# Kernel tuning notes

Measured on AMD Instinct MI355X. Metric: run time of the kernel, lower is better.

## Reference

```python
import jax, jax.numpy as jnp
import numpy as np

L, D, H, V, T_BLK, B, T = 6, 768, 12, 32000, 1024, 4, 1024
HD = D // H          # head size = 64
FF = 4 * D           # FFN hidden
EPS = 1e-5


def _ln(x, g, b):
    m = x.mean(-1, keepdims=True)
    v = ((x - m) ** 2).mean(-1, keepdims=True)
    return (x - m) * jax.lax.rsqrt(v + EPS) * g + b


def _attn(q_in, kv_in, wqkv, wo, bo, causal):
    # wqkv: [3, D, D]; heads batched (equivalent to concat of per-head Linear outputs)
    Bq, Tq, _ = q_in.shape
    Tk = kv_in.shape[1]
    q = (q_in @ wqkv[0]).reshape(Bq, Tq, H, HD)
    k = (kv_in @ wqkv[1]).reshape(Bq, Tk, H, HD)
    v = (kv_in @ wqkv[2]).reshape(Bq, Tk, H, HD)
    wei = jnp.einsum('bqhd,bkhd->bhqk', q, k) * (HD ** -0.5)
    if causal:
        mask = jnp.tril(jnp.ones((Tq, Tk), dtype=bool))
        wei = jnp.where(mask, wei, -jnp.inf)
    wei = jax.nn.softmax(wei, axis=-1)
    out = jnp.einsum('bhqk,bkhd->bqhd', wei, v).reshape(Bq, Tq, D)
    return out @ wo + bo


def _ffn(x, w1, b1, w2, b2):
    return jax.nn.relu(x @ w1 + b1) @ w2 + b2


def _forward(idx, encoder_input,
             enc_tok, enc_pos, enc_qkv, enc_wo, enc_bo, enc_w1, enc_b1, enc_w2, enc_b2,
             enc_ln1g, enc_ln1b, enc_ln2g, enc_ln2b, enc_lnfg, enc_lnfb,
             dec_tok, dec_pos, dec_qkv, dec_wo, dec_bo, dec_cqkv, dec_cwo, dec_cbo,
             dec_w1, dec_b1, dec_w2, dec_b2,
             dec_ln1g, dec_ln1b, dec_ln2g, dec_ln2b, dec_ln3g, dec_ln3b,
             dec_lnfg, dec_lnfb, lm_w, lm_b):
    # ---- encoder (NOTE: original Head always applies causal tril, so encoder is causal) ----
    Te = encoder_input.shape[1]
    x = enc_tok[encoder_input] + enc_pos[:Te]
    for i in range(L):
        h = _ln(x, enc_ln1g[i], enc_ln1b[i])
        x = x + _attn(h, h, enc_qkv[i], enc_wo[i], enc_bo[i], causal=True)
        h = _ln(x, enc_ln2g[i], enc_ln2b[i])
        x = x + _ffn(h, enc_w1[i], enc_b1[i], enc_w2[i], enc_b2[i])
    enc_out = _ln(x, enc_lnfg, enc_lnfb)
    # ---- decoder ----
    Td = idx.shape[1]
    y = dec_tok[idx] + dec_pos[:Td]
    for i in range(L):
        h = _ln(y, dec_ln1g[i], dec_ln1b[i])
        y = y + _attn(h, h, dec_qkv[i], dec_wo[i], dec_bo[i], causal=True)
        h = _ln(y, dec_ln2g[i], dec_ln2b[i])
        y = y + _attn(h, enc_out, dec_cqkv[i], dec_cwo[i], dec_cbo[i], causal=False)
        h = _ln(y, dec_ln3g[i], dec_ln3b[i])
        y = y + _ffn(h, dec_w1[i], dec_b1[i], dec_w2[i], dec_b2[i])
    y = _ln(y, dec_lnfg, dec_lnfb)
    return y @ lm_w + lm_b  # logits [B, T, V]


def setup_inputs() -> dict:
    key = jax.random.key(0)
    keys = iter(jax.random.split(key, 80))
    def nrm(shape, s=0.02):
        return jax.random.normal(next(keys), shape, dtype=jnp.float32) * s
    z = lambda shape: jnp.zeros(shape, jnp.float32)
    o = lambda shape: jnp.ones(shape, jnp.float32)
    inp = {}
    inp['idx'] = jax.random.randint(next(keys), (B, T), 0, V)
    inp['encoder_input'] = jax.random.randint(next(keys), (B, T), 0, V)
    # encoder params
    inp['enc_tok'] = nrm((V, D)); inp['enc_pos'] = nrm((T_BLK, D))
    inp['enc_qkv'] = nrm((L, 3, D, D)); inp['enc_wo'] = nrm((L, D, D)); inp['enc_bo'] = z((L, D))
    inp['enc_w1'] = nrm((L, D, FF)); inp['enc_b1'] = z((L, FF))
    inp['enc_w2'] = nrm((L, FF, D)); inp['enc_b2'] = z((L, D))
    inp['enc_ln1g'] = o((L, D)); inp['enc_ln1b'] = z((L, D))
    inp['enc_ln2g'] = o((L, D)); inp['enc_ln2b'] = z((L, D))
    inp['enc_lnfg'] = o((D,)); inp['enc_lnfb'] = z((D,))
    # decoder params
    inp['dec_tok'] = nrm((V, D)); inp['dec_pos'] = nrm((T_BLK, D))
    inp['dec_qkv'] = nrm((L, 3, D, D)); inp['dec_wo'] = nrm((L, D, D)); inp['dec_bo'] = z((L, D))
    inp['dec_cqkv'] = nrm((L, 3, D, D)); inp['dec_cwo'] = nrm((L, D, D)); inp['dec_cbo'] = z((L, D))
    inp['dec_w1'] = nrm((L, D, FF)); inp['dec_b1'] = z((L, FF))
    inp['dec_w2'] = nrm((L, FF, D)); inp['dec_b2'] = z((L, D))
    inp['dec_ln1g'] = o((L, D)); inp['dec_ln1b'] = z((L, D))
    inp['dec_ln2g'] = o((L, D)); inp['dec_ln2b'] = z((L, D))
    inp['dec_ln3g'] = o((L, D)); inp['dec_ln3b'] = z((L, D))
    inp['dec_lnfg'] = o((D,)); inp['dec_lnfb'] = z((D,))
    inp['lm_w'] = nrm((D, V)); inp['lm_b'] = z((V,))
    return inp


def reference(idx, encoder_input,
              enc_tok, enc_pos, enc_qkv, enc_wo, enc_bo, enc_w1, enc_b1, enc_w2, enc_b2,
              enc_ln1g, enc_ln1b, enc_ln2g, enc_ln2b, enc_lnfg, enc_lnfb,
              dec_tok, dec_pos, dec_qkv, dec_wo, dec_bo, dec_cqkv, dec_cwo, dec_cbo,
              dec_w1, dec_b1, dec_w2, dec_b2,
              dec_ln1g, dec_ln1b, dec_ln2g, dec_ln2b, dec_ln3g, dec_ln3b,
              dec_lnfg, dec_lnfb, lm_w, lm_b):
    return _forward(idx, encoder_input,
                    enc_tok, enc_pos, enc_qkv, enc_wo, enc_bo, enc_w1, enc_b1, enc_w2, enc_b2,
                    enc_ln1g, enc_ln1b, enc_ln2g, enc_ln2b, enc_lnfg, enc_lnfb,
                    dec_tok, dec_pos, dec_qkv, dec_wo, dec_bo, dec_cqkv, dec_cwo, dec_cbo,
                    dec_w1, dec_b1, dec_w2, dec_b2,
                    dec_ln1g, dec_ln1b, dec_ln2g, dec_ln2b, dec_ln3g, dec_ln3b,
                    dec_lnfg, dec_lnfb, lm_w, lm_b)
```

## Files before the change

kernel.cpp:

```cpp
#include <hip/hip_runtime.h>


typedef __bf16 bf16x8 __attribute__((ext_vector_type(8)));
typedef float  f32x4  __attribute__((ext_vector_type(4)));
typedef unsigned short u16x4 __attribute__((ext_vector_type(4)));
typedef unsigned short u16x8 __attribute__((ext_vector_type(8)));

constexpr int Lc = 6, Dc = 768, Hc = 12, HDc = 64, Vc = 32000;
constexpr int Bc = 4, Tc = 1024, FFc = 3072;
constexpr int Mtot = Bc * Tc;

static __device__ __forceinline__ unsigned short f2bf(float f) {
  union { float f; unsigned u; } x; x.f = f;
  unsigned r = x.u + 0x7fffu + ((x.u >> 16) & 1u);
  return (unsigned short)(r >> 16);
}
static __device__ __forceinline__ float bf2f(unsigned short s) {
  union { unsigned u; float f; } c; c.u = (unsigned)s << 16; return c.f;
}

static __device__ __forceinline__ void gl_lds16(const unsigned short* g, unsigned short* l) {
  __builtin_amdgcn_global_load_lds(
      (const __attribute__((address_space(1))) unsigned int*)g,
      (__attribute__((address_space(3))) unsigned int*)l, 16, 0, 0);
}

template <int N> static __device__ __forceinline__ void wait_vm() {
  if constexpr (N == 0)      asm volatile("s_waitcnt vmcnt(0)" ::: "memory");
  else if constexpr (N == 3) asm volatile("s_waitcnt vmcnt(3)" ::: "memory");
  else if constexpr (N == 4) asm volatile("s_waitcnt vmcnt(4)" ::: "memory");
}

static __device__ __forceinline__ float blockReduceSum(float v, float* red) {
  #pragma unroll
  for (int o = 32; o; o >>= 1) v += __shfl_xor(v, o, 64);
  int w = threadIdx.x >> 6;
  __syncthreads();
  if ((threadIdx.x & 63) == 0) red[w] = v;
  __syncthreads();
  return red[0] + red[1] + red[2] + red[3];
}

__global__ __launch_bounds__(256) void wconv_k(const float* __restrict__ W,
                                               unsigned short* __restrict__ WT,
                                               int K, int N) {
  __shared__ float t[32][33];
  const long zoff = (long)blockIdx.z * K * N;
  const int k0 = blockIdx.x * 32, n0 = blockIdx.y * 32;
  const int tid = threadIdx.x;
  const int rr = tid >> 3;
  const int cc = (tid & 7) * 4;
  f32x4 v = *reinterpret_cast<const f32x4*>(W + zoff + (long)(k0 + rr) * N + n0 + cc);
  #pragma unroll
  for (int j = 0; j < 4; j++) t[rr][cc + j] = v[j];
  __syncthreads();
  u16x4 o;
  #pragma unroll
  for (int j = 0; j < 4; j++) o[j] = f2bf(t[cc + j][rr]);
  *reinterpret_cast<u16x4*>(WT + zoff + (long)(n0 + rr) * K + k0 + cc) = o;
}

__global__ __launch_bounds__(256) void vtrans_k(const unsigned short* __restrict__ V,
                                                unsigned short* __restrict__ VT) {
  __shared__ unsigned short t[64][65];
  const int bh = blockIdx.y;
  const int b = bh / Hc, h = bh % Hc;
  const int t0 = blockIdx.x * 64;
  const int tid = threadIdx.x;
  const int rr = tid >> 3;
  const int c8 = (tid & 7) * 8;
  #pragma unroll
  for (int rep = 0; rep < 2; rep++) {
    int row = rep * 32 + rr;
    u16x8 v = *reinterpret_cast<const u16x8*>(V + (long)(b * Tc + t0 + row) * Dc + h * HDc + c8);
    #pragma unroll
    for (int j = 0; j < 8; j++) t[row][c8 + j] = v[j];
  }
  __syncthreads();
  #pragma unroll
  for (int rep = 0; rep < 2; rep++) {
    int hd = rep * 32 + rr;
    u16x8 o;
    #pragma unroll
    for (int j = 0; j < 8; j++) o[j] = t[c8 + j][hd];
    *reinterpret_cast<u16x8*>(VT + ((long)bh * HDc + hd) * Tc + t0 + c8) = o;
  }
}

__global__ __launch_bounds__(256) void embed_k(const int* __restrict__ idx,
                                               const float* __restrict__ tok,
                                               const float* __restrict__ pos,
                                               float* __restrict__ out) {
  const long row = blockIdx.x;
  const int t = (int)(row % Tc);
  const long id = idx[row];
  #pragma unroll
  for (int j = 0; j < 3; j++) {
    int e = threadIdx.x + j * 256;
    out[row * Dc + e] = tok[id * Dc + e] + pos[(long)t * Dc + e];
  }
}

__global__ __launch_bounds__(256) void ln_k(const float* __restrict__ X,
                                            const float* __restrict__ g,
                                            const float* __restrict__ bta,
                                            unsigned short* __restrict__ out) {
  __shared__ float red[4];
  const long row = blockIdx.x;
  const int tid = threadIdx.x;
  float v[3];
  #pragma unroll
  for (int j = 0; j < 3; j++) v[j] = X[row * Dc + tid + j * 256];
  float s = v[0] + v[1] + v[2];
  s = blockReduceSum(s, red);
  float mean = s * (1.f / 768.f);
  float q = 0.f;
  #pragma unroll
  for (int j = 0; j < 3; j++) { float d = v[j] - mean; q += d * d; }
  q = blockReduceSum(q, red);
  float rstd = rsqrtf(q * (1.f / 768.f) + 1e-5f);
  #pragma unroll
  for (int j = 0; j < 3; j++) {
    int e = tid + j * 256;
    out[row * Dc + e] = f2bf((v[j] - mean) * rstd * g[e] + bta[e]);
  }
}

template <bool CAUSAL>
__global__ __launch_bounds__(256) void flash_k(
    const unsigned short* __restrict__ Q,
    const unsigned short* __restrict__ K,
    const unsigned short* __restrict__ VT,
    unsigned short* __restrict__ O) {
  __shared__ __align__(16) unsigned short Ks[128 * 64];
  __shared__ __align__(16) unsigned short Vs[64 * 128];
  __shared__ __align__(16) unsigned short Ps[4][32 * 128];

  const int tid = threadIdx.x;
  const int lane = tid & 63;
  const int w = tid >> 6;
  const int lane16 = lane & 15;
  const int l4 = lane >> 4;
  const int bh = blockIdx.y;
  const int b = bh / Hc, h = bh % Hc;
  const int q0 = blockIdx.x * 128;

  const unsigned short* Qb = Q + ((long)b * Tc) * Dc + h * HDc;
  const unsigned short* Kb = K + ((long)b * Tc) * Dc + h * HDc;
  const unsigned short* Vb = VT + (long)bh * HDc * Tc;
  unsigned short* Ob = O + ((long)b * Tc) * Dc + h * HDc;

  bf16x8 qf[2][2];
  #pragma unroll
  for (int m = 0; m < 2; m++)
    #pragma unroll
    for (int kk = 0; kk < 2; kk++) {
      u16x8 raw = *reinterpret_cast<const u16x8*>(
          Qb + (long)(q0 + w * 32 + m * 16 + lane16) * Dc + kk * 32 + l4 * 8);
      bf16x8 f;
      #pragma unroll
      for (int j = 0; j < 8; j++) f[j] = (__bf16)(bf2f(raw[j]) * 0.125f);
      qf[m][kk] = f;
    }

  float mrow[2][4], lrow[2][4];
  f32x4 accO[2][4];
  #pragma unroll
  for (int m = 0; m < 2; m++)
    #pragma unroll
    for (int r = 0; r < 4; r++) { mrow[m][r] = -1e30f; lrow[m][r] = 0.f; }
  #pragma unroll
  for (int m = 0; m < 2; m++)
    #pragma unroll
    for (int d4 = 0; d4 < 4; d4++)
      #pragma unroll
      for (int r = 0; r < 4; r++) accO[m][d4][r] = 0.f;

  const int nch = CAUSAL ? (blockIdx.x + 1) : (Tc / 128);
  for (int c = 0; c < nch; c++) {
    const int k0 = c * 128;
    __syncthreads();
    #pragma unroll
    for (int it = 0; it < 4; it++) {
      int u = (it * 4 + w) * 64 + lane;
      int r = u >> 3, s = u & 7;
      gl_lds16(Kb + (long)(k0 + r) * Dc + ((s ^ (r & 7)) * 8), &Ks[(it * 4 + w) * 512]);
      int r2 = u >> 4, s2 = u & 15;
      gl_lds16(Vb + (long)r2 * Tc + k0 + ((s2 ^ (r2 & 7)) * 8), &Vs[(it * 4 + w) * 512]);
    }
    __syncthreads();

    f32x4 sacc[2][8];
    #pragma unroll
    for (int m = 0; m < 2; m++)
      #pragma unroll
      for (int n = 0; n < 8; n++)
        #pragma unroll
        for (int r = 0; r < 4; r++) sacc[m][n][r] = 0.f;
    #pragma unroll
    for (int n = 0; n < 8; n++) {
      int row = n * 16 + lane16;
      #pragma unroll
      for (int kk = 0; kk < 2; kk++) {
        bf16x8 kf = *reinterpret_cast<const bf16x8*>(
            &Ks[row * 64 + (((kk * 4 + l4) ^ (row & 7)) * 8)]);
        sacc[0][n] = __builtin_amdgcn_mfma_f32_16x16x32_bf16(qf[0][kk], kf, sacc[0][n], 0, 0, 0);
        sacc[1][n] = __builtin_amdgcn_mfma_f32_16x16x32_bf16(qf[1][kk], kf, sacc[1][n], 0, 0, 0);
      }
    }

    if (CAUSAL && c == nch - 1) {
      #pragma unroll
      for (int m = 0; m < 2; m++)
        #pragma unroll
        for (int n = 0; n < 8; n++)
          #pragma unroll
          for (int r = 0; r < 4; r++) {
            int kcol = k0 + n * 16 + lane16;
            int q = q0 + w * 32 + m * 16 + l4 * 4 + r;
            if (kcol > q) sacc[m][n][r] = -1e30f;
          }
    }

    #pragma unroll
    for (int m = 0; m < 2; m++)
      #pragma unroll
      for (int r = 0; r < 4; r++) {
        float smax = sacc[m][0][r];
        #pragma unroll
        for (int n = 1; n < 8; n++) smax = fmaxf(smax, sacc[m][n][r]);
        #pragma unroll
        for (int off = 1; off < 16; off <<= 1) smax = fmaxf(smax, __shfl_xor(smax, off, 64));
        float mold = mrow[m][r];
        float mnew = fmaxf(mold, smax);
        float sc = __expf(mold - mnew);
        float psum = 0.f;
        unsigned short pv[8];
        #pragma unroll
        for (int n = 0; n < 8; n++) {
          float p = __expf(sacc[m][n][r] - mnew);
          psum += p;
          pv[n] = f2bf(p);
        }
        #pragma unroll
        for (int off = 1; off < 16; off <<= 1) psum += __shfl_xor(psum, off, 64);
        lrow[m][r] = lrow[m][r] * sc + psum;
        mrow[m][r] = mnew;
        #pragma unroll
        for (int d4 = 0; d4 < 4; d4++) accO[m][d4][r] *= sc;
        int prow = m * 16 + l4 * 4 + r;
        #pragma unroll
        for (int n = 0; n < 8; n++) {
          int col = n * 16 + lane16;
          Ps[w][prow * 128 + (((col >> 3) ^ (prow & 7)) * 8) + (col & 7)] = pv[n];
        }
      }

    #pragma unroll
    for (int kk = 0; kk < 4; kk++) {
      bf16x8 pa[2];
      #pragma unroll
      for (int m = 0; m < 2; m++) {
        int arow = m * 16 + lane16;
        pa[m] = *reinterpret_cast<const bf16x8*>(
            &Ps[w][arow * 128 + (((kk * 4 + l4) ^ (arow & 7)) * 8)]);
      }
      #pragma unroll
      for (int d4 = 0; d4 < 4; d4++) {
        int vrow = d4 * 16 + lane16;
        bf16x8 vf = *reinterpret_cast<const bf16x8*>(
            &Vs[vrow * 128 + (((kk * 4 + l4) ^ (vrow & 7)) * 8)]);
        accO[0][d4] = __builtin_amdgcn_mfma_f32_16x16x32_bf16(pa[0], vf, accO[0][d4], 0, 0, 0);
        accO[1][d4] = __builtin_amdgcn_mfma_f32_16x16x32_bf16(pa[1], vf, accO[1][d4], 0, 0, 0);
      }
    }
  }

  #pragma unroll
  for (int m = 0; m < 2; m++)
    #pragma unroll
    for (int r = 0; r < 4; r++) {
      float inv = 1.f / lrow[m][r];
      int q = q0 + w * 32 + m * 16 + l4 * 4 + r;
      #pragma unroll
      for (int d4 = 0; d4 < 4; d4++)
        Ob[(long)q * Dc + d4 * 16 + lane16] = f2bf(accO[m][d4][r] * inv);
    }
}

template <int BM, int BN, int MF, int NF, int MINW,
          bool HASBIAS, bool RELU, bool HASRES, bool OUTBF>
__global__ __launch_bounds__(256, MINW) void gemm_k(
    const unsigned short* __restrict__ A, long sAb, long sAh, int lda,
    const unsigned short* __restrict__ BT, long sBb, long sBh, int ldb,
    void* Cp, long sCb, long sCh, int ldc,
    const float* __restrict__ bias,
    const float* __restrict__ Res, int ldr,
    int K, int nH, float alpha) {
  constexpr int AI = BM / 64;
  constexpr int BI = BN / 64;
  constexpr int VC = AI + BI;
  __shared__ __align__(16) unsigned short As[2][BM * 32];
  __shared__ __align__(16) unsigned short Bs[2][BN * 32];

  const int tid = threadIdx.x;
  const int lane = tid & 63;
  const int w = tid >> 6;
  const int wr = w >> 1, wc = w & 1;
  const int lane16 = lane & 15;
  const int l4 = lane >> 4;

  const int z = blockIdx.z;
  const int bb = z / nH, hh = z % nH;
  const long offA = sAb * bb + sAh * hh;
  const long offB = sBb * bb + sBh * hh;
  const long offC = sCb * bb + sCh * hh;

  const int gx = gridDim.x;
  const int nwg = gx * gridDim.y;
  const int id = blockIdx.y * gx + blockIdx.x;
  const int q8 = nwg >> 3, r8 = nwg & 7;
  const int xcd = id & 7, ord = id >> 3;
  const int swz = (xcd < r8 ? xcd * (q8 + 1) : r8 * (q8 + 1) + (xcd - r8) * q8) + ord;
  const int m0 = (swz % gx) * BM;
  const int n0 = (swz / gx) * BN;

  const int srow = lane >> 2;
  const int sslot = ((lane & 3) ^ ((srow >> 1) & 3)) * 8;

  const unsigned short* aP[AI];
  #pragma unroll
  for (int j = 0; j < AI; j++)
    aP[j] = A + offA + (long)(m0 + w * (BM / 4) + j * 16 + srow) * lda + sslot;
  const unsigned short* bP[BI];
  #pragma unroll
  for (int j = 0; j < BI; j++)
    bP[j] = BT + offB + (long)(n0 + w * (BN / 4) + j * 16 + srow) * ldb + sslot;

  f32x4 acc[MF][NF];
  #pragma unroll
  for (int m = 0; m < MF; m++)
    #pragma unroll
    for (int n = 0; n < NF; n++)
      #pragma unroll
      for (int r = 0; r < 4; r++) acc[m][n][r] = 0.f;

  auto STAGE = [&](int buf, int k0) {
    #pragma unroll
    for (int j = 0; j < AI; j++)
      gl_lds16(aP[j] + k0, &As[buf][(w * (BM / 4) + j * 16) * 32]);
    #pragma unroll
    for (int j = 0; j < BI; j++)
      gl_lds16(bP[j] + k0, &Bs[buf][(w * (BN / 4) + j * 16) * 32]);
  };

  const int nt = K / 32;
  STAGE(0, 0);
  int cur = 0;
  for (int t = 0; t < nt; t++) {
    if (t + 1 < nt) { STAGE(cur ^ 1, (t + 1) * 32); wait_vm<VC>(); }
    else            { wait_vm<0>(); }
    __builtin_amdgcn_sched_barrier(0);
    __builtin_amdgcn_s_barrier();
    __builtin_amdgcn_sched_barrier(0);

    bf16x8 afr[MF], bfr[NF];
    #pragma unroll
    for (int n = 0; n < NF; n++) {
      int row = wc * NF * 16 + n * 16 + lane16;
      bfr[n] = *reinterpret_cast<const bf16x8*>(
          &Bs[cur][row * 32 + ((l4 ^ ((row >> 1) & 3)) * 8)]);
    }
    #pragma unroll
    for (int m = 0; m < MF; m++) {
      int row = wr * MF * 16 + m * 16 + lane16;
      afr[m] = *reinterpret_cast<const bf16x8*>(
          &As[cur][row * 32 + ((l4 ^ ((row >> 1) & 3)) * 8)]);
    }
    __builtin_amdgcn_s_setprio(1);
    #pragma unroll
    for (int m = 0; m < MF; m++)
      #pragma unroll
      for (int n = 0; n < NF; n++)
        acc[m][n] = __builtin_amdgcn_mfma_f32_16x16x32_bf16(afr[m], bfr[n], acc[m][n], 0, 0, 0);
    __builtin_amdgcn_s_setprio(0);

    asm volatile("s_waitcnt lgkmcnt(0)" ::: "memory");
    __builtin_amdgcn_sched_barrier(0);
    __builtin_amdgcn_s_barrier();
    cur ^= 1;
  }

  const int r0 = m0 + wr * MF * 16;
  const int c0 = n0 + wc * NF * 16;
  #pragma unroll
  for (int m = 0; m < MF; m++) {
    #pragma unroll
    for (int n = 0; n < NF; n++) {
      #pragma unroll
      for (int r = 0; r < 4; r++) {
        int rr = r0 + m * 16 + l4 * 4 + r;
        int cc = c0 + n * 16 + lane16;
        float v = acc[m][n][r] * alpha;
        if constexpr (HASBIAS) v += bias[cc];
        if constexpr (RELU) v = fmaxf(v, 0.f);
        if constexpr (HASRES) v += Res[offC + (long)rr * ldr + cc];
        if constexpr (OUTBF) ((unsigned short*)Cp)[offC + (long)rr * ldc + cc] = f2bf(v);
        else                 ((float*)Cp)[offC + (long)rr * ldc + cc] = v;
      }
    }
  }
}

extern "C" void kernel_launch(void* const* d_in, const int* in_sizes, int n_in,
                              void* d_out, int out_size, void* d_ws, size_t ws_size,
                              hipStream_t stream) {
  (void)in_sizes; (void)n_in; (void)out_size;

  const int*   idx      = (const int*)d_in[0];
  const int*   enc_in   = (const int*)d_in[1];
  const float* enc_tok  = (const float*)d_in[2];
  const float* enc_pos  = (const float*)d_in[3];
  const float* enc_qkv  = (const float*)d_in[4];
  const float* enc_wo   = (const float*)d_in[5];
  const float* enc_bo   = (const float*)d_in[6];
  const float* enc_w1   = (const float*)d_in[7];
  const float* enc_b1   = (const float*)d_in[8];
  const float* enc_w2   = (const float*)d_in[9];
  const float* enc_b2   = (const float*)d_in[10];
  const float* enc_ln1g = (const float*)d_in[11];
  const float* enc_ln1b = (const float*)d_in[12];
  const float* enc_ln2g = (const float*)d_in[13];
  const float* enc_ln2b = (const float*)d_in[14];
  const float* enc_lnfg = (const float*)d_in[15];
  const float* enc_lnfb = (const float*)d_in[16];
  const float* dec_tok  = (const float*)d_in[17];
  const float* dec_pos  = (const float*)d_in[18];
  const float* dec_qkv  = (const float*)d_in[19];
  const float* dec_wo   = (const float*)d_in[20];
  const float* dec_bo   = (const float*)d_in[21];
  const float* dec_cqkv = (const float*)d_in[22];
  const float* dec_cwo  = (const float*)d_in[23];
  const float* dec_cbo  = (const float*)d_in[24];
  const float* dec_w1   = (const float*)d_in[25];
  const float* dec_b1   = (const float*)d_in[26];
  const float* dec_w2   = (const float*)d_in[27];
  const float* dec_b2   = (const float*)d_in[28];
  const float* dec_ln1g = (const float*)d_in[29];
  const float* dec_ln1b = (const float*)d_in[30];
  const float* dec_ln2g = (const float*)d_in[31];
  const float* dec_ln2b = (const float*)d_in[32];
  const float* dec_ln3g = (const float*)d_in[33];
  const float* dec_ln3b = (const float*)d_in[34];
  const float* dec_lnfg = (const float*)d_in[35];
  const float* dec_lnfb = (const float*)d_in[36];
  const float* lm_w     = (const float*)d_in[37];
  const float* lm_b     = (const float*)d_in[38];

  constexpr long De2 = (long)Dc * Dc;
  constexpr long DF  = (long)Dc * FFc;

  unsigned short* wcache = (unsigned short*)d_out;
  size_t woff = 0;
  auto take = [&](size_t n) { unsigned short* p = wcache + woff; woff += n; return p; };
  unsigned short* enc_qkvT  = take(18ul * De2);
  unsigned short* enc_woT   = take(6ul * De2);
  unsigned short* enc_w1T   = take(6ul * DF);
  unsigned short* enc_w2T   = take(6ul * DF);
  unsigned short* dec_qkvT  = take(18ul * De2);
  unsigned short* dec_woT   = take(6ul * De2);
  unsigned short* dec_cqkvT = take(18ul * De2);
  unsigned short* dec_cwoT  = take(6ul * De2);
  unsigned short* dec_w1T   = take(6ul * DF);
  unsigned short* dec_w2T   = take(6ul * DF);

  char* ws = (char*)d_ws;
  const size_t need = (size_t)Dc * Vc * 2 + 2ull * Mtot * Dc * 4 + 3ull * Mtot * Dc * 2 +
                      3ull * Mtot * Dc * 2 + (size_t)Mtot * FFc * 2 + (size_t)Mtot * Dc * 2 +
                      (size_t)Bc * Hc * HDc * Tc * 2 + 4096;
  if (ws_size < need) return;
  auto takeW = [&](size_t bytes) { char* p = ws; ws += (bytes + 255) & ~255ull; return p; };
  unsigned short* lm_wT = (unsigned short*)takeW((size_t)Dc * Vc * 2);
  float* xe             = (float*)takeW((size_t)Mtot * Dc * 4);
  float* xd             = (float*)takeW((size_t)Mtot * Dc * 4);
  unsigned short* hbf   = (unsigned short*)takeW((size_t)Mtot * Dc * 2);
  unsigned short* qkvb  = (unsigned short*)takeW(3ull * Mtot * Dc * 2);
  unsigned short* ao    = (unsigned short*)takeW((size_t)Mtot * Dc * 2);
  unsigned short* mid   = (unsigned short*)takeW((size_t)Mtot * FFc * 2);
  unsigned short* eo    = (unsigned short*)takeW((size_t)Mtot * Dc * 2);
  unsigned short* vT    = (unsigned short*)takeW((size_t)Bc * Hc * HDc * Tc * 2);
  unsigned short* qb = qkvb;
  unsigned short* kb = qkvb + (size_t)Mtot * Dc;
  unsigned short* vb = qkvb + 2ull * Mtot * Dc;

  const dim3 TB(256);

  wconv_k<<<dim3(Dc/32, Dc/32, 18), TB, 0, stream>>>(enc_qkv, enc_qkvT, Dc, Dc);
  wconv_k<<<dim3(Dc/32, Dc/32,  6), TB, 0, stream>>>(enc_wo,  enc_woT,  Dc, Dc);
  wconv_k<<<dim3(Dc/32, FFc/32, 6), TB, 0, stream>>>(enc_w1,  enc_w1T,  Dc, FFc);
  wconv_k<<<dim3(FFc/32, Dc/32, 6), TB, 0, stream>>>(enc_w2,  enc_w2T,  FFc, Dc);
  wconv_k<<<dim3(Dc/32, Dc/32, 18), TB, 0, stream>>>(dec_qkv, dec_qkvT, Dc, Dc);
  wconv_k<<<dim3(Dc/32, Dc/32,  6), TB, 0, stream>>>(dec_wo,  dec_woT,  Dc, Dc);
  wconv_k<<<dim3(Dc/32, Dc/32, 18), TB, 0, stream>>>(dec_cqkv,dec_cqkvT,Dc, Dc);
  wconv_k<<<dim3(Dc/32, Dc/32,  6), TB, 0, stream>>>(dec_cwo, dec_cwoT, Dc, Dc);
  wconv_k<<<dim3(Dc/32, FFc/32, 6), TB, 0, stream>>>(dec_w1,  dec_w1T,  Dc, FFc);
  wconv_k<<<dim3(FFc/32, Dc/32, 6), TB, 0, stream>>>(dec_w2,  dec_w2T,  FFc, Dc);
  wconv_k<<<dim3(Dc/32, Vc/32,  1), TB, 0, stream>>>(lm_w,    lm_wT,    Dc, Vc);

  auto LN = [&](const float* X, const float* g, const float* b, unsigned short* o) {
    ln_k<<<dim3(Mtot), TB, 0, stream>>>(X, g, b, o);
  };
  auto QKV3 = [&](const unsigned short* Abf, const unsigned short* W3T) {
    gemm_k<128,128,4,4,3,false,false,false,true><<<dim3(Mtot/128, Dc/128, 3), TB, 0, stream>>>(
        Abf, 0, 0, Dc, W3T, De2, 0, Dc,
        qkvb, (long)Mtot*Dc, 0, Dc, nullptr, nullptr, 0, Dc, 1, 1.f);
  };
  auto PROJ1 = [&](const unsigned short* Abf, const unsigned short* WT, unsigned short* Cb) {
    gemm_k<128,64,4,2,4,false,false,false,true><<<dim3(Mtot/128, Dc/64, 1), TB, 0, stream>>>(
        Abf, 0, 0, Dc, WT, 0, 0, Dc,
        Cb, 0, 0, Dc, nullptr, nullptr, 0, Dc, 1, 1.f);
  };
  auto KV2 = [&](const unsigned short* Abf, const unsigned short* W2T) {
    gemm_k<128,64,4,2,4,false,false,false,true><<<dim3(Mtot/128, Dc/64, 2), TB, 0, stream>>>(
        Abf, 0, 0, Dc, W2T, De2, 0, Dc,
        kb, (long)Mtot*Dc, 0, Dc, nullptr, nullptr, 0, Dc, 1, 1.f);
  };
  auto VT = [&]() {
    vtrans_k<<<dim3(Tc/64, Bc*Hc), TB, 0, stream>>>(vb, vT);
  };
  auto FLASH = [&](bool causal) {
    if (causal) flash_k<true ><<<dim3(Tc/128, Bc*Hc), TB, 0, stream>>>(qb, kb, vT, ao);
    else        flash_k<false><<<dim3(Tc/128, Bc*Hc), TB, 0, stream>>>(qb, kb, vT, ao);
  };
  auto ORES = [&](const unsigned short* Abf, const unsigned short* WT, const float* bias, float* X) {
    gemm_k<128,64,4,2,4,true,false,true,false><<<dim3(Mtot/128, Dc/64, 1), TB, 0, stream>>>(
        Abf, 0, 0, Dc, WT, 0, 0, Dc,
        X, 0, 0, Dc, bias, X, Dc, Dc, 1, 1.f);
  };
  auto FFN1 = [&](const unsigned short* Abf, const unsigned short* WT, const float* bias) {
    gemm_k<128,128,4,4,3,true,true,false,true><<<dim3(Mtot/128, FFc/128, 1), TB, 0, stream>>>(
        Abf, 0, 0, Dc, WT, 0, 0, Dc,
        mid, 0, 0, FFc, bias, nullptr, 0, Dc, 1, 1.f);
  };
  auto FFN2 = [&](const unsigned short* WT, const float* bias, float* X) {
    gemm_k<128,64,4,2,4,true,false,true,false><<<dim3(Mtot/128, Dc/64, 1), TB, 0, stream>>>(
        mid, 0, 0, FFc, WT, 0, 0, FFc,
        X, 0, 0, Dc, bias, X, Dc, FFc, 1, 1.f);
  };

  embed_k<<<dim3(Mtot), TB, 0, stream>>>(enc_in, enc_tok, enc_pos, xe);
  for (int i = 0; i < Lc; i++) {
    LN(xe, enc_ln1g + i * Dc, enc_ln1b + i * Dc, hbf);
    QKV3(hbf, enc_qkvT + (size_t)i * 3 * De2);
    VT(); FLASH(true);
    ORES(ao, enc_woT + (size_t)i * De2, enc_bo + i * Dc, xe);
    LN(xe, enc_ln2g + i * Dc, enc_ln2b + i * Dc, hbf);
    FFN1(hbf, enc_w1T + (size_t)i * DF, enc_b1 + i * FFc);
    FFN2(enc_w2T + (size_t)i * DF, enc_b2 + i * Dc, xe);
  }
  LN(xe, enc_lnfg, enc_lnfb, eo);

  embed_k<<<dim3(Mtot), TB, 0, stream>>>(idx, dec_tok, dec_pos, xd);
  for (int i = 0; i < Lc; i++) {
    LN(xd, dec_ln1g + i * Dc, dec_ln1b + i * Dc, hbf);
    QKV3(hbf, dec_qkvT + (size_t)i * 3 * De2);
    VT(); FLASH(true);
    ORES(ao, dec_woT + (size_t)i * De2, dec_bo + i * Dc, xd);
    LN(xd, dec_ln2g + i * Dc, dec_ln2b + i * Dc, hbf);
    PROJ1(hbf, dec_cqkvT + (size_t)i * 3 * De2, qb);
    KV2(eo, dec_cqkvT + (size_t)i * 3 * De2 + De2);
    VT(); FLASH(false);
    ORES(ao, dec_cwoT + (size_t)i * De2, dec_cbo + i * Dc, xd);
    LN(xd, dec_ln3g + i * Dc, dec_ln3b + i * Dc, hbf);
    FFN1(hbf, dec_w1T + (size_t)i * DF, dec_b1 + i * FFc);
    FFN2(dec_w2T + (size_t)i * DF, dec_b2 + i * Dc, xd);
  }
  LN(xd, dec_lnfg, dec_lnfb, hbf);

  gemm_k<128,128,4,4,3,true,false,false,false><<<dim3(Mtot/128, Vc/128, 1), TB, 0, stream>>>(
      hbf, 0, 0, Dc, lm_wT, 0, 0, Dc,
      d_out, 0, 0, Vc, lm_b, nullptr, 0, Dc, 1, 1.f);
}
```

Before: 4.025 ms.

## Merge cross-attention Q/KV GEMMs, shrink GEMM tiles, nontemporal LM-head stores

```diff
diff --git a/kernel.cpp b/kernel.cpp
--- a/kernel.cpp
+++ b/kernel.cpp
@@ -27,6 +27,7 @@
 
 template <int N> static __device__ __forceinline__ void wait_vm() {
   if constexpr (N == 0)      asm volatile("s_waitcnt vmcnt(0)" ::: "memory");
+  else if constexpr (N == 2) asm volatile("s_waitcnt vmcnt(2)" ::: "memory");
   else if constexpr (N == 3) asm volatile("s_waitcnt vmcnt(3)" ::: "memory");
   else if constexpr (N == 4) asm volatile("s_waitcnt vmcnt(4)" ::: "memory");
 }
@@ -289,13 +290,14 @@
 }
 
 template <int BM, int BN, int MF, int NF, int MINW,
-          bool HASBIAS, bool RELU, bool HASRES, bool OUTBF>
+          bool HASBIAS, bool RELU, bool HASRES, bool OUTBF, bool NT>
 __global__ __launch_bounds__(256, MINW) void gemm_k(
     const unsigned short* __restrict__ A, long sAb, long sAh, int lda,
     const unsigned short* __restrict__ BT, long sBb, long sBh, int ldb,
     void* Cp, long sCb, long sCh, int ldc,
     const float* __restrict__ bias,
     const float* __restrict__ Res, int ldr,
+    const unsigned short* __restrict__ A2,
     int K, int nH, float alpha) {
   constexpr int AI = BM / 64;
   constexpr int BI = BN / 64;
@@ -312,6 +314,7 @@
 
   const int z = blockIdx.z;
   const int bb = z / nH, hh = z % nH;
+  const unsigned short* Abase = (A2 != nullptr && hh != 0) ? A2 : A;
   const long offA = sAb * bb + sAh * hh;
   const long offB = sBb * bb + sBh * hh;
   const long offC = sCb * bb + sCh * hh;
@@ -331,7 +334,7 @@
   const unsigned short* aP[AI];
   #pragma unroll
   for (int j = 0; j < AI; j++)
-    aP[j] = A + offA + (long)(m0 + w * (BM / 4) + j * 16 + srow) * lda + sslot;
+    aP[j] = Abase + offA + (long)(m0 + w * (BM / 4) + j * 16 + srow) * lda + sslot;
   const unsigned short* bP[BI];
   #pragma unroll
   for (int j = 0; j < BI; j++)
@@ -405,8 +408,13 @@
         if constexpr (HASBIAS) v += bias[cc];
         if constexpr (RELU) v = fmaxf(v, 0.f);
         if constexpr (HASRES) v += Res[offC + (long)rr * ldr + cc];
-        if constexpr (OUTBF) ((unsigned short*)Cp)[offC + (long)rr * ldc + cc] = f2bf(v);
-        else                 ((float*)Cp)[offC + (long)rr * ldc + cc] = v;
+        if constexpr (OUTBF) {
+          ((unsigned short*)Cp)[offC + (long)rr * ldc + cc] = f2bf(v);
+        } else {
+          float* dst = (float*)Cp + offC + (long)rr * ldc + cc;
+          if constexpr (NT) __builtin_nontemporal_store(v, dst);
+          else              *dst = v;
+        }
       }
     }
   }
@@ -511,19 +519,16 @@
     ln_k<<<dim3(Mtot), TB, 0, stream>>>(X, g, b, o);
   };
   auto QKV3 = [&](const unsigned short* Abf, const unsigned short* W3T) {
-    gemm_k<128,128,4,4,3,false,false,false,true><<<dim3(Mtot/128, Dc/128, 3), TB, 0, stream>>>(
-        Abf, 0, 0, Dc, W3T, De2, 0, Dc,
-        qkvb, (long)Mtot*Dc, 0, Dc, nullptr, nullptr, 0, Dc, 1, 1.f);
-  };
-  auto PROJ1 = [&](const unsigned short* Abf, const unsigned short* WT, unsigned short* Cb) {
-    gemm_k<128,64,4,2,4,false,false,false,true><<<dim3(Mtot/128, Dc/64, 1), TB, 0, stream>>>(
-        Abf, 0, 0, Dc, WT, 0, 0, Dc,
-        Cb, 0, 0, Dc, nullptr, nullptr, 0, Dc, 1, 1.f);
-  };
-  auto KV2 = [&](const unsigned short* Abf, const unsigned short* W2T) {
-    gemm_k<128,64,4,2,4,false,false,false,true><<<dim3(Mtot/128, Dc/64, 2), TB, 0, stream>>>(
-        Abf, 0, 0, Dc, W2T, De2, 0, Dc,
-        kb, (long)Mtot*Dc, 0, Dc, nullptr, nullptr, 0, Dc, 1, 1.f);
+    gemm_k<128,64,4,2,4,false,false,false,true,false>
+      <<<dim3(Mtot/128, Dc/64, 3), TB, 0, stream>>>(
+        Abf, De2 * 0 + 0, 0, Dc, W3T, De2, 0, Dc,
+        qkvb, (long)Mtot*Dc, 0, Dc, nullptr, nullptr, 0, nullptr, Dc, 1, 1.f);
+  };
+  auto CQKV = [&](const unsigned short* Abf, const unsigned short* WcT) {
+    gemm_k<64,64,2,2,4,false,false,false,true,false>
+      <<<dim3(Mtot/64, Dc/64, 3), TB, 0, stream>>>(
+        Abf, 0, 0, Dc, WcT, 0, De2, Dc,
+        qkvb, 0, (long)Mtot*Dc, Dc, nullptr, nullptr, 0, eo, Dc, 3, 1.f);
   };
   auto VT = [&]() {
     vtrans_k<<<dim3(Tc/64, Bc*Hc), TB, 0, stream>>>(vb, vT);
@@ -533,19 +538,22 @@
     else        flash_k<false><<<dim3(Tc/128, Bc*Hc), TB, 0, stream>>>(qb, kb, vT, ao);
   };
   auto ORES = [&](const unsigned short* Abf, const unsigned short* WT, const float* bias, float* X) {
-    gemm_k<128,64,4,2,4,true,false,true,false><<<dim3(Mtot/128, Dc/64, 1), TB, 0, stream>>>(
+    gemm_k<64,64,2,2,4,true,false,true,false,false>
+      <<<dim3(Mtot/64, Dc/64, 1), TB, 0, stream>>>(
         Abf, 0, 0, Dc, WT, 0, 0, Dc,
-        X, 0, 0, Dc, bias, X, Dc, Dc, 1, 1.f);
+        X, 0, 0, Dc, bias, X, Dc, nullptr, Dc, 1, 1.f);
   };
   auto FFN1 = [&](const unsigned short* Abf, const unsigned short* WT, const float* bias) {
-    gemm_k<128,128,4,4,3,true,true,false,true><<<dim3(Mtot/128, FFc/128, 1), TB, 0, stream>>>(
+    gemm_k<128,128,4,4,3,true,true,false,true,false>
+      <<<dim3(Mtot/128, FFc/128, 1), TB, 0, stream>>>(
         Abf, 0, 0, Dc, WT, 0, 0, Dc,
-        mid, 0, 0, FFc, bias, nullptr, 0, Dc, 1, 1.f);
+        mid, 0, 0, FFc, bias, nullptr, 0, nullptr, Dc, 1, 1.f);
   };
   auto FFN2 = [&](const unsigned short* WT, const float* bias, float* X) {
-    gemm_k<128,64,4,2,4,true,false,true,false><<<dim3(Mtot/128, Dc/64, 1), TB, 0, stream>>>(
+    gemm_k<64,64,2,2,4,true,false,true,false,false>
+      <<<dim3(Mtot/64, Dc/64, 1), TB, 0, stream>>>(
         mid, 0, 0, FFc, WT, 0, 0, FFc,
-        X, 0, 0, Dc, bias, X, Dc, FFc, 1, 1.f);
+        X, 0, 0, Dc, bias, X, Dc, nullptr, FFc, 1, 1.f);
   };
 
   embed_k<<<dim3(Mtot), TB, 0, stream>>>(enc_in, enc_tok, enc_pos, xe);
@@ -567,8 +575,7 @@
     VT(); FLASH(true);
     ORES(ao, dec_woT + (size_t)i * De2, dec_bo + i * Dc, xd);
     LN(xd, dec_ln2g + i * Dc, dec_ln2b + i * Dc, hbf);
-    PROJ1(hbf, dec_cqkvT + (size_t)i * 3 * De2, qb);
-    KV2(eo, dec_cqkvT + (size_t)i * 3 * De2 + De2);
+    CQKV(hbf, dec_cqkvT + (size_t)i * 3 * De2);
     VT(); FLASH(false);
     ORES(ao, dec_cwoT + (size_t)i * De2, dec_cbo + i * Dc, xd);
     LN(xd, dec_ln3g + i * Dc, dec_ln3b + i * Dc, hbf);
@@ -577,7 +584,8 @@
   }
   LN(xd, dec_lnfg, dec_lnfb, hbf);
 
-  gemm_k<128,128,4,4,3,true,false,false,false><<<dim3(Mtot/128, Vc/128, 1), TB, 0, stream>>>(
+  gemm_k<128,128,4,4,3,true,false,false,false,true>
+    <<<dim3(Mtot/128, Vc/128, 1), TB, 0, stream>>>(
       hbf, 0, 0, Dc, lm_wT, 0, 0, Dc,
-      d_out, 0, 0, Vc, lm_b, nullptr, 0, Dc, 1, 1.f);
-}
+      d_out, 0, 0, Vc, lm_b, nullptr, 0, nullptr, Dc, 1, 1.f);
+}
```

Result: no change. 3.990 ms (-0.9%).
